# Kernel optimization log

Measured on AMD Instinct MI355X. Metric: run time of the kernel, lower is better.

The kernel has to match this reference:

```python
import jax, jax.numpy as jnp
import numpy as np

BLOCK_SIZE = 16
# Signed NVFP4 (e2m1) value table; code = sign_bit<<3 | magnitude_index
FP4_VALUES = jnp.array(
    [0.0, 0.5, 1.0, 1.5, 2.0, 3.0, 4.0, 6.0,
     -0.0, -0.5, -1.0, -1.5, -2.0, -3.0, -4.0, -6.0],
    dtype=jnp.float32)


def setup_inputs() -> dict:
    key = jax.random.key(0)
    k1, k2, k3 = jax.random.split(key, 3)
    O, I = 4096, 4096
    x = jax.random.normal(k1, (2, 1024, I), dtype=jnp.float32)
    # per-block scales (positive), one per 16-element block along in_features
    weight_scales = jax.random.uniform(k2, (O, I // BLOCK_SIZE), dtype=jnp.float32,
                                       minval=0.01, maxval=1.0)
    weight_q = jax.random.randint(k3, (O, I), 0, 16, dtype=jnp.int32)
    return {"x": x, "weight_scales": weight_scales, "weight_q": weight_q}


def dequantize_nvfp4_sim(weight_q, weight_scales, block_size=BLOCK_SIZE):
    O, I = weight_q.shape
    vals = FP4_VALUES[weight_q]                              # [O, I] fp32 e2m1 values
    w = vals.reshape(O, I // block_size, block_size) * weight_scales[:, :, None]
    return w.reshape(O, I)


def reference(x, weight_scales, weight_q):
    # Dequantize NVFP4 -> BF16, then BF16 GEMM (F.linear), cast back to input dtype.
    w = dequantize_nvfp4_sim(weight_q, weight_scales).astype(jnp.bfloat16)  # [O, I]
    x_bf16 = x.astype(jnp.bfloat16)
    out = jnp.einsum('bsi,oi->bso', x_bf16, w)               # [B, S, O] bf16
    return out.astype(x.dtype)
```

## Files before the change

kernel.cpp:

```cpp
#include <hip/hip_runtime.h>

typedef __bf16  bf16x8 __attribute__((ext_vector_type(8)));
typedef float   f32x4  __attribute__((ext_vector_type(4)));
typedef short   short8 __attribute__((ext_vector_type(8)));

static __device__ __forceinline__ unsigned short f2bf(float f) {
  union { float f; unsigned int u; } v; v.f = f;
  unsigned int u = v.u;
  u += 0x7fffu + ((u >> 16) & 1u);
  return (unsigned short)(u >> 16);
}

static __device__ __forceinline__ float fp4_decode(int qc) {
  int e = (qc >> 1) & 3;
  float m = (float)(qc & 1);
  float mag = (e == 0) ? (0.5f * m)
                       : ((2.0f + m) * 0.5f * (float)(1 << (e - 1)));
  return (qc & 8) ? -mag : mag;
}

__global__ __launch_bounds__(256) void w4a16_prep(
    const int* __restrict__ wq, const float* __restrict__ wsc,
    short* __restrict__ wout, int nblkW,
    const float* __restrict__ x, short* __restrict__ xb, int n8) {
  const int nbW = nblkW >> 8;
  if ((int)blockIdx.x < nbW) {
    int idx = blockIdx.x * 256 + threadIdx.x;
    if (idx >= nblkW) return;
    float s = wsc[idx];
    const int4* qp = (const int4*)wq + (size_t)idx * 4;
    int4 q0 = qp[0], q1 = qp[1], q2 = qp[2], q3 = qp[3];
    short8 r0, r1;
    r0[0] = (short)f2bf(fp4_decode(q0.x) * s);
    r0[1] = (short)f2bf(fp4_decode(q0.y) * s);
    r0[2] = (short)f2bf(fp4_decode(q0.z) * s);
    r0[3] = (short)f2bf(fp4_decode(q0.w) * s);
    r0[4] = (short)f2bf(fp4_decode(q1.x) * s);
    r0[5] = (short)f2bf(fp4_decode(q1.y) * s);
    r0[6] = (short)f2bf(fp4_decode(q1.z) * s);
    r0[7] = (short)f2bf(fp4_decode(q1.w) * s);
    r1[0] = (short)f2bf(fp4_decode(q2.x) * s);
    r1[1] = (short)f2bf(fp4_decode(q2.y) * s);
    r1[2] = (short)f2bf(fp4_decode(q2.z) * s);
    r1[3] = (short)f2bf(fp4_decode(q2.w) * s);
    r1[4] = (short)f2bf(fp4_decode(q3.x) * s);
    r1[5] = (short)f2bf(fp4_decode(q3.y) * s);
    r1[6] = (short)f2bf(fp4_decode(q3.z) * s);
    r1[7] = (short)f2bf(fp4_decode(q3.w) * s);
    short8* op = (short8*)wout + (size_t)idx * 2;
    op[0] = r0;
    op[1] = r1;
  } else {
    int idx = (blockIdx.x - nbW) * 256 + threadIdx.x;
    if (idx >= n8) return;
    const float4* xp = (const float4*)x + (size_t)idx * 2;
    float4 a = xp[0], b = xp[1];
    short8 r;
    r[0] = (short)f2bf(a.x); r[1] = (short)f2bf(a.y);
    r[2] = (short)f2bf(a.z); r[3] = (short)f2bf(a.w);
    r[4] = (short)f2bf(b.x); r[5] = (short)f2bf(b.y);
    r[6] = (short)f2bf(b.z); r[7] = (short)f2bf(b.w);
    ((short8*)xb)[idx] = r;
  }
}

#define BM 128
#define BN 256
#define BK 64
#define NBUF 3
#define ASZ (BM * BK)
#define BSZ (BN * BK)

__global__ __launch_bounds__(512, 2) void w4a16_gemm_1ph(
    const short* __restrict__ A, const short* __restrict__ B,
    float* __restrict__ C, int M, int N, int K) {
  __shared__ __attribute__((aligned(16))) short As[NBUF * ASZ];
  __shared__ __attribute__((aligned(16))) short Bs[NBUF * BSZ];

  const int tid  = threadIdx.x;
  const int lane = tid & 63;
  const int wid  = tid >> 6;
  const int wr   = wid >> 2;
  const int wc   = wid & 3;

  const int bm = blockIdx.y * BM;
  const int bn = blockIdx.x * BN;

  f32x4 acc[4][4] = {};

  const int fr    = lane & 15;
  const int klane = lane >> 4;
  const int xv    = fr & 7;

  const size_t rowbytes = (size_t)K * 2;

  size_t aoff[2];  int aldso[2];
#pragma unroll
  for (int r = 0; r < 2; ++r) {
    int u = r * 512 + tid;
    int row = u >> 3, c = u & 7;
    int csrc = c ^ (row & 7);
    aoff[r]  = (size_t)(bm + row) * rowbytes + (size_t)csrc * 16;
    aldso[r] = u * 16;
  }
  size_t boff[4];  int bldso[4];
#pragma unroll
  for (int r = 0; r < 4; ++r) {
    int u = r * 512 + tid;
    int row = u >> 3, c = u & 7;
    int csrc = c ^ (row & 7);
    boff[r]  = (size_t)(bn + row) * rowbytes + (size_t)csrc * 16;
    bldso[r] = u * 16;
  }

  const char* Ag = (const char*)A;
  const char* Bg = (const char*)B;

#define STAGE_A(bufbase, koff2, r)                                              \
  __builtin_amdgcn_global_load_lds(                                             \
      (const __attribute__((address_space(1))) unsigned int*)(Ag + aoff[r] + (koff2)), \
      (__attribute__((address_space(3))) unsigned int*)((char*)(bufbase) + aldso[r]),  \
      16, 0, 0)
#define STAGE_B(bufbase, koff2, r)                                              \
  __builtin_amdgcn_global_load_lds(                                             \
      (const __attribute__((address_space(1))) unsigned int*)(Bg + boff[r] + (koff2)), \
      (__attribute__((address_space(3))) unsigned int*)((char*)(bufbase) + bldso[r]),  \
      16, 0, 0)

  auto readA = [&](const short* Ab, int mq, int mi, int kk) -> bf16x8 {
    int row = wr * 64 + mq * 32 + mi * 16 + fr;
    int c = kk * 4 + klane;
    return *(const bf16x8*)((const char*)Ab + (size_t)row * 128 + ((c ^ xv) << 4));
  };
  auto readB = [&](const short* Bb, int ni, int kk) -> bf16x8 {
    int row = wc * 64 + ni * 16 + fr;
    int c = kk * 4 + klane;
    return *(const bf16x8*)((const char*)Bb + (size_t)row * 128 + ((c ^ xv) << 4));
  };

  const int NT = K / BK;

  {
    char* A0 = (char*)As; char* B0 = (char*)Bs;
    char* A1 = (char*)(As + ASZ); char* B1 = (char*)(Bs + BSZ);
    STAGE_A(A0, 0, 0); STAGE_A(A0, 0, 1);
    STAGE_B(B0, 0, 0); STAGE_B(B0, 0, 1); STAGE_B(B0, 0, 2); STAGE_B(B0, 0, 3);
    size_t k2 = (size_t)BK * 2;
    STAGE_A(A1, k2, 0); STAGE_A(A1, k2, 1);
    STAGE_B(B1, k2, 0); STAGE_B(B1, k2, 1); STAGE_B(B1, k2, 2); STAGE_B(B1, k2, 3);
  }
  asm volatile("s_waitcnt vmcnt(6)");
  __builtin_amdgcn_s_barrier();

  int cur = 0, nxt = 2;
  for (int t = 0; t < NT; ++t) {
    const short* Ab = As + cur * ASZ;
    const short* Bb = Bs + cur * BSZ;
    char* An = (char*)(As + nxt * ASZ);
    char* Bn = (char*)(Bs + nxt * BSZ);
    const size_t koff2 = (size_t)(t + 2) * (BK * 2);
    const bool pf = (t + 2) < NT;

    bf16x8 af0[2][2], bfr[4][2], af1[2][2];

#pragma unroll
    for (int mi = 0; mi < 2; ++mi)
#pragma unroll
      for (int kk = 0; kk < 2; ++kk)
        af0[mi][kk] = readA(Ab, 0, mi, kk);
#pragma unroll
    for (int ni = 0; ni < 4; ++ni)
#pragma unroll
      for (int kk = 0; kk < 2; ++kk)
        bfr[ni][kk] = readB(Bb, ni, kk);
#pragma unroll
    for (int mi = 0; mi < 2; ++mi)
#pragma unroll
      for (int kk = 0; kk < 2; ++kk)
        af1[mi][kk] = readA(Ab, 1, mi, kk);

    if (pf) {
      STAGE_A(An, koff2, 0); STAGE_A(An, koff2, 1);
      STAGE_B(Bn, koff2, 0); STAGE_B(Bn, koff2, 1);
      STAGE_B(Bn, koff2, 2); STAGE_B(Bn, koff2, 3);
    }

    __builtin_amdgcn_s_setprio(1);
#pragma unroll
    for (int mi = 0; mi < 2; ++mi)
#pragma unroll
      for (int ni = 0; ni < 4; ++ni)
#pragma unroll
        for (int kk = 0; kk < 2; ++kk)
          acc[mi][ni] = __builtin_amdgcn_mfma_f32_16x16x32_bf16(
              af0[mi][kk], bfr[ni][kk], acc[mi][ni], 0, 0, 0);
#pragma unroll
    for (int mi = 0; mi < 2; ++mi)
#pragma unroll
      for (int ni = 0; ni < 4; ++ni)
#pragma unroll
        for (int kk = 0; kk < 2; ++kk)
          acc[2 + mi][ni] = __builtin_amdgcn_mfma_f32_16x16x32_bf16(
              af1[mi][kk], bfr[ni][kk], acc[2 + mi][ni], 0, 0, 0);
    __builtin_amdgcn_s_setprio(0);

    if (t < NT - 1) {
      __builtin_amdgcn_sched_barrier(0);
      if (pf) asm volatile("s_waitcnt vmcnt(6)");
      else    asm volatile("s_waitcnt vmcnt(0)");
    }
    __builtin_amdgcn_s_barrier();

    cur = (cur == NBUF - 1) ? 0 : cur + 1;
    nxt = (nxt == NBUF - 1) ? 0 : nxt + 1;
  }

  const int cn = lane & 15;
  const int rb = (lane >> 4) * 4;
#pragma unroll
  for (int ai = 0; ai < 4; ++ai)
#pragma unroll
    for (int bj = 0; bj < 4; ++bj) {
      int m0 = bm + wr * 64 + ai * 16 + rb;
      int n0 = bn + wc * 64 + bj * 16 + cn;
#pragma unroll
      for (int r = 0; r < 4; ++r)
        C[(size_t)(m0 + r) * N + n0] = acc[ai][bj][r];
    }
}

extern "C" void kernel_launch(void* const* d_in, const int* in_sizes, int n_in,
                              void* d_out, int out_size, void* d_ws, size_t ws_size,
                              hipStream_t stream) {
  const float* x   = (const float*)d_in[0];
  const float* wsc = (const float*)d_in[1];
  const int*   wq  = (const int*)d_in[2];
  float* out = (float*)d_out;

  const int K = 4096;
  const int N = in_sizes[2] / K;
  const int M = in_sizes[0] / K;

  short* Wb = (short*)d_ws;
  short* Xb = Wb + (size_t)N * K;

  int nblkW = (N * K) / 16;
  int n8    = (M * K) / 8;
  int gridP = (nblkW >> 8) + ((n8 + 255) >> 8);
  w4a16_prep<<<gridP, 256, 0, stream>>>(wq, wsc, Wb, nblkW, x, Xb, n8);

  dim3 grid(N / BN, M / BM);
  w4a16_gemm_1ph<<<grid, 512, 0, stream>>>(Xb, Wb, out, M, N, K);
}
```

Measured before the change: 90.93 us.

## Load A fragments directly into registers and double-buffer only B in LDS

The activation operand A is no longer staged through shared memory. Each wave loads its A fragments straight from global memory into registers, ping-ponging between two register sets one tile ahead. Only the weight operand B stays in LDS, now double-buffered instead of triple-buffered, and the main loop is unrolled by two to alternate buffers. This saves LDS traffic and capacity for A, at the cost of redundant A loads across the four waves that share rows, poorly coalesced 16-byte row-strided global reads, shallower B prefetch, and higher register pressure.

Result: slower. 179.2 us (+97.1%).

```diff
diff --git a/kernel.cpp b/kernel.cpp
--- a/kernel.cpp
+++ b/kernel.cpp
@@ -67,15 +67,12 @@
 #define BM 128
 #define BN 256
 #define BK 64
-#define NBUF 3
-#define ASZ (BM * BK)
 #define BSZ (BN * BK)
 
-__global__ __launch_bounds__(512, 2) void w4a16_gemm_1ph(
+__global__ __launch_bounds__(512, 2) void w4a16_gemm_areg(
     const short* __restrict__ A, const short* __restrict__ B,
     float* __restrict__ C, int M, int N, int K) {
-  __shared__ __attribute__((aligned(16))) short As[NBUF * ASZ];
-  __shared__ __attribute__((aligned(16))) short Bs[NBUF * BSZ];
+  __shared__ __attribute__((aligned(16))) short Bs[2 * BSZ];
 
   const int tid  = threadIdx.x;
   const int lane = tid & 63;
@@ -94,15 +91,6 @@
 
   const size_t rowbytes = (size_t)K * 2;
 
-  size_t aoff[2];  int aldso[2];
-#pragma unroll
-  for (int r = 0; r < 2; ++r) {
-    int u = r * 512 + tid;
-    int row = u >> 3, c = u & 7;
-    int csrc = c ^ (row & 7);
-    aoff[r]  = (size_t)(bm + row) * rowbytes + (size_t)csrc * 16;
-    aldso[r] = u * 16;
-  }
   size_t boff[4];  int bldso[4];
 #pragma unroll
   for (int r = 0; r < 4; ++r) {
@@ -112,26 +100,21 @@
     boff[r]  = (size_t)(bn + row) * rowbytes + (size_t)csrc * 16;
     bldso[r] = u * 16;
   }
-
-  const char* Ag = (const char*)A;
   const char* Bg = (const char*)B;
 
-#define STAGE_A(bufbase, koff2, r)                                              \
-  __builtin_amdgcn_global_load_lds(                                             \
-      (const __attribute__((address_space(1))) unsigned int*)(Ag + aoff[r] + (koff2)), \
-      (__attribute__((address_space(3))) unsigned int*)((char*)(bufbase) + aldso[r]),  \
-      16, 0, 0)
 #define STAGE_B(bufbase, koff2, r)                                              \
   __builtin_amdgcn_global_load_lds(                                             \
       (const __attribute__((address_space(1))) unsigned int*)(Bg + boff[r] + (koff2)), \
       (__attribute__((address_space(3))) unsigned int*)((char*)(bufbase) + bldso[r]),  \
       16, 0, 0)
 
-  auto readA = [&](const short* Ab, int mq, int mi, int kk) -> bf16x8 {
-    int row = wr * 64 + mq * 32 + mi * 16 + fr;
-    int c = kk * 4 + klane;
-    return *(const bf16x8*)((const char*)Ab + (size_t)row * 128 + ((c ^ xv) << 4));
-  };
+  const char* Apl[4];
+#pragma unroll
+  for (int mi = 0; mi < 4; ++mi) {
+    int row = bm + wr * 64 + mi * 16 + fr;
+    Apl[mi] = (const char*)A + (size_t)row * rowbytes + klane * 16;
+  }
+
   auto readB = [&](const short* Bb, int ni, int kk) -> bf16x8 {
     int row = wc * 64 + ni * 16 + fr;
     int c = kk * 4 + klane;
@@ -139,80 +122,56 @@
   };
 
   const int NT = K / BK;
-
-  {
-    char* A0 = (char*)As; char* B0 = (char*)Bs;
-    char* A1 = (char*)(As + ASZ); char* B1 = (char*)(Bs + BSZ);
-    STAGE_A(A0, 0, 0); STAGE_A(A0, 0, 1);
-    STAGE_B(B0, 0, 0); STAGE_B(B0, 0, 1); STAGE_B(B0, 0, 2); STAGE_B(B0, 0, 3);
-    size_t k2 = (size_t)BK * 2;
-    STAGE_A(A1, k2, 0); STAGE_A(A1, k2, 1);
-    STAGE_B(B1, k2, 0); STAGE_B(B1, k2, 1); STAGE_B(B1, k2, 2); STAGE_B(B1, k2, 3);
-  }
-  asm volatile("s_waitcnt vmcnt(6)");
+  short* Bs0 = Bs;
+  short* Bs1 = Bs + BSZ;
+
+  bf16x8 bfr[4][2], afA[4][2], afB[4][2];
+
+  STAGE_B(Bs0, 0, 0); STAGE_B(Bs0, 0, 1); STAGE_B(Bs0, 0, 2); STAGE_B(Bs0, 0, 3);
+  __builtin_amdgcn_sched_barrier(0);
+#pragma unroll
+  for (int mi = 0; mi < 4; ++mi)
+#pragma unroll
+    for (int kk = 0; kk < 2; ++kk)
+      afA[mi][kk] = *(const bf16x8*)(Apl[mi] + kk * 64);
+  __builtin_amdgcn_sched_barrier(0);
+  asm volatile("s_waitcnt vmcnt(8)");
   __builtin_amdgcn_s_barrier();
 
-  int cur = 0, nxt = 2;
-  for (int t = 0; t < NT; ++t) {
-    const short* Ab = As + cur * ASZ;
-    const short* Bb = Bs + cur * BSZ;
-    char* An = (char*)(As + nxt * ASZ);
-    char* Bn = (char*)(Bs + nxt * BSZ);
-    const size_t koff2 = (size_t)(t + 2) * (BK * 2);
-    const bool pf = (t + 2) < NT;
-
-    bf16x8 af0[2][2], bfr[4][2], af1[2][2];
-
-#pragma unroll
-    for (int mi = 0; mi < 2; ++mi)
-#pragma unroll
-      for (int kk = 0; kk < 2; ++kk)
-        af0[mi][kk] = readA(Ab, 0, mi, kk);
-#pragma unroll
-    for (int ni = 0; ni < 4; ++ni)
-#pragma unroll
-      for (int kk = 0; kk < 2; ++kk)
-        bfr[ni][kk] = readB(Bb, ni, kk);
-#pragma unroll
-    for (int mi = 0; mi < 2; ++mi)
-#pragma unroll
-      for (int kk = 0; kk < 2; ++kk)
-        af1[mi][kk] = readA(Ab, 1, mi, kk);
-
-    if (pf) {
-      STAGE_A(An, koff2, 0); STAGE_A(An, koff2, 1);
-      STAGE_B(Bn, koff2, 0); STAGE_B(Bn, koff2, 1);
-      STAGE_B(Bn, koff2, 2); STAGE_B(Bn, koff2, 3);
-    }
-
-    __builtin_amdgcn_s_setprio(1);
-#pragma unroll
-    for (int mi = 0; mi < 2; ++mi)
-#pragma unroll
-      for (int ni = 0; ni < 4; ++ni)
-#pragma unroll
-        for (int kk = 0; kk < 2; ++kk)
-          acc[mi][ni] = __builtin_amdgcn_mfma_f32_16x16x32_bf16(
-              af0[mi][kk], bfr[ni][kk], acc[mi][ni], 0, 0, 0);
-#pragma unroll
-    for (int mi = 0; mi < 2; ++mi)
-#pragma unroll
-      for (int ni = 0; ni < 4; ++ni)
-#pragma unroll
-        for (int kk = 0; kk < 2; ++kk)
-          acc[2 + mi][ni] = __builtin_amdgcn_mfma_f32_16x16x32_bf16(
-              af1[mi][kk], bfr[ni][kk], acc[2 + mi][ni], 0, 0, 0);
-    __builtin_amdgcn_s_setprio(0);
-
-    if (t < NT - 1) {
-      __builtin_amdgcn_sched_barrier(0);
-      if (pf) asm volatile("s_waitcnt vmcnt(6)");
-      else    asm volatile("s_waitcnt vmcnt(0)");
-    }
-    __builtin_amdgcn_s_barrier();
-
-    cur = (cur == NBUF - 1) ? 0 : cur + 1;
-    nxt = (nxt == NBUF - 1) ? 0 : nxt + 1;
+#define TILE_BODY(t_, CURB, NXTB, AFU, AFL)                                     \
+  do {                                                                          \
+    _Pragma("unroll") for (int ni = 0; ni < 4; ++ni)                            \
+      _Pragma("unroll") for (int kk = 0; kk < 2; ++kk)                          \
+        bfr[ni][kk] = readB((CURB), ni, kk);                                    \
+    const bool pf_ = (t_) + 1 < NT;                                             \
+    if (pf_) {                                                                  \
+      const size_t ko_ = (size_t)((t_) + 1) * (BK * 2);                         \
+      STAGE_B((NXTB), ko_, 0); STAGE_B((NXTB), ko_, 1);                         \
+      STAGE_B((NXTB), ko_, 2); STAGE_B((NXTB), ko_, 3);                         \
+    }                                                                           \
+    __builtin_amdgcn_sched_barrier(0);  \
+    if (pf_) {                                                                  \
+      _Pragma("unroll") for (int mi = 0; mi < 4; ++mi)                          \
+        _Pragma("unroll") for (int kk = 0; kk < 2; ++kk)                        \
+          AFL[mi][kk] = *(const bf16x8*)(Apl[mi] + ((t_) + 1) * 128 + kk * 64); \
+    }                                                                           \
+    __builtin_amdgcn_s_setprio(1);                                              \
+    _Pragma("unroll") for (int mi = 0; mi < 4; ++mi)                            \
+      _Pragma("unroll") for (int ni = 0; ni < 4; ++ni)                          \
+        _Pragma("unroll") for (int kk = 0; kk < 2; ++kk)                        \
+          acc[mi][ni] = __builtin_amdgcn_mfma_f32_16x16x32_bf16(                \
+              AFU[mi][kk], bfr[ni][kk], acc[mi][ni], 0, 0, 0);                  \
+    __builtin_amdgcn_s_setprio(0);                                              \
+    if ((t_) < NT - 1) {                                                        \
+      __builtin_amdgcn_sched_barrier(0);                                        \
+      asm volatile("s_waitcnt vmcnt(8)");    \
+      __builtin_amdgcn_s_barrier();                                             \
+    }                                                                           \
+  } while (0)
+
+  for (int t = 0; t < NT; t += 2) {
+    TILE_BODY(t,     Bs0, Bs1, afA, afB);
+    TILE_BODY(t + 1, Bs1, Bs0, afB, afA);
   }
 
   const int cn = lane & 15;
@@ -250,5 +209,5 @@
   w4a16_prep<<<gridP, 256, 0, stream>>>(wq, wsc, Wb, nblkW, x, Xb, n8);
 
   dim3 grid(N / BN, M / BM);
-  w4a16_gemm_1ph<<<grid, 512, 0, stream>>>(Xb, Wb, out, M, N, K);
-}
+  w4a16_gemm_areg<<<grid, 512, 0, stream>>>(Xb, Wb, out, M, N, K);
+}
```

## Shrink GEMM tiles to 128x128x32 with 4 waves for higher occupancy

Applied to the files above, without the earlier changes.

Reduces the GEMM block tile from 128x256x64 with 8 waves to 128x128x32 with 4 waves, targeting three blocks per CU instead of two. The LDS swizzle and fragment-read pattern are rewritten for 64-byte rows, and each K step now issues 16 MFMAs per wave instead of 32. This is meant to raise occupancy and produce more blocks to fill the CUs, at the cost of less data reuse per tile, twice as many barriers per K, and more global traffic for A.

Measured after the change: 101.3 us. +11.5%, slower.

```diff
diff --git a/kernel.cpp b/kernel.cpp
--- a/kernel.cpp
+++ b/kernel.cpp
@@ -65,13 +65,13 @@
 }
 
 #define BM 128
-#define BN 256
-#define BK 64
+#define BN 128
+#define BK 32
 #define NBUF 3
 #define ASZ (BM * BK)
 #define BSZ (BN * BK)
 
-__global__ __launch_bounds__(512, 2) void w4a16_gemm_1ph(
+__global__ __launch_bounds__(256, 3) void w4a16_gemm_occ(
     const short* __restrict__ A, const short* __restrict__ B,
     float* __restrict__ C, int M, int N, int K) {
   __shared__ __attribute__((aligned(16))) short As[NBUF * ASZ];
@@ -80,8 +80,8 @@
   const int tid  = threadIdx.x;
   const int lane = tid & 63;
   const int wid  = tid >> 6;
-  const int wr   = wid >> 2;
-  const int wc   = wid & 3;
+  const int wr   = wid >> 1;
+  const int wc   = wid & 1;
 
   const int bm = blockIdx.y * BM;
   const int bn = blockIdx.x * BN;
@@ -90,66 +90,55 @@
 
   const int fr    = lane & 15;
   const int klane = lane >> 4;
-  const int xv    = fr & 7;
+  const int xk    = klane ^ ((fr >> 1) & 3);
 
   const size_t rowbytes = (size_t)K * 2;
 
-  size_t aoff[2];  int aldso[2];
+  size_t aoff[2], boff[2];  int ldso[2];
 #pragma unroll
   for (int r = 0; r < 2; ++r) {
-    int u = r * 512 + tid;
-    int row = u >> 3, c = u & 7;
-    int csrc = c ^ (row & 7);
-    aoff[r]  = (size_t)(bm + row) * rowbytes + (size_t)csrc * 16;
-    aldso[r] = u * 16;
-  }
-  size_t boff[4];  int bldso[4];
-#pragma unroll
-  for (int r = 0; r < 4; ++r) {
-    int u = r * 512 + tid;
-    int row = u >> 3, c = u & 7;
-    int csrc = c ^ (row & 7);
-    boff[r]  = (size_t)(bn + row) * rowbytes + (size_t)csrc * 16;
-    bldso[r] = u * 16;
-  }
-
+    int u = r * 256 + tid;
+    int row = u >> 2, c = u & 3;
+    int csrc = c ^ ((row >> 1) & 3);
+    aoff[r] = (size_t)(bm + row) * rowbytes + (size_t)csrc * 16;
+    boff[r] = (size_t)(bn + row) * rowbytes + (size_t)csrc * 16;
+    ldso[r] = u * 16;
+  }
   const char* Ag = (const char*)A;
   const char* Bg = (const char*)B;
 
 #define STAGE_A(bufbase, koff2, r)                                              \
   __builtin_amdgcn_global_load_lds(                                             \
       (const __attribute__((address_space(1))) unsigned int*)(Ag + aoff[r] + (koff2)), \
-      (__attribute__((address_space(3))) unsigned int*)((char*)(bufbase) + aldso[r]),  \
+      (__attribute__((address_space(3))) unsigned int*)((char*)(bufbase) + ldso[r]),   \
       16, 0, 0)
 #define STAGE_B(bufbase, koff2, r)                                              \
   __builtin_amdgcn_global_load_lds(                                             \
       (const __attribute__((address_space(1))) unsigned int*)(Bg + boff[r] + (koff2)), \
-      (__attribute__((address_space(3))) unsigned int*)((char*)(bufbase) + bldso[r]),  \
+      (__attribute__((address_space(3))) unsigned int*)((char*)(bufbase) + ldso[r]),   \
       16, 0, 0)
 
-  auto readA = [&](const short* Ab, int mq, int mi, int kk) -> bf16x8 {
-    int row = wr * 64 + mq * 32 + mi * 16 + fr;
-    int c = kk * 4 + klane;
-    return *(const bf16x8*)((const char*)Ab + (size_t)row * 128 + ((c ^ xv) << 4));
+  auto readA = [&](const short* Ab, int mi) -> bf16x8 {
+    int row = wr * 64 + mi * 16 + fr;
+    return *(const bf16x8*)((const char*)Ab + (size_t)row * 64 + (xk << 4));
   };
-  auto readB = [&](const short* Bb, int ni, int kk) -> bf16x8 {
+  auto readB = [&](const short* Bb, int ni) -> bf16x8 {
     int row = wc * 64 + ni * 16 + fr;
-    int c = kk * 4 + klane;
-    return *(const bf16x8*)((const char*)Bb + (size_t)row * 128 + ((c ^ xv) << 4));
+    return *(const bf16x8*)((const char*)Bb + (size_t)row * 64 + (xk << 4));
   };
 
   const int NT = K / BK;
 
   {
-    char* A0 = (char*)As; char* B0 = (char*)Bs;
-    char* A1 = (char*)(As + ASZ); char* B1 = (char*)(Bs + BSZ);
+    char* A0 = (char*)As;            char* B0 = (char*)Bs;
+    char* A1 = (char*)(As + ASZ);    char* B1 = (char*)(Bs + BSZ);
     STAGE_A(A0, 0, 0); STAGE_A(A0, 0, 1);
-    STAGE_B(B0, 0, 0); STAGE_B(B0, 0, 1); STAGE_B(B0, 0, 2); STAGE_B(B0, 0, 3);
+    STAGE_B(B0, 0, 0); STAGE_B(B0, 0, 1);
     size_t k2 = (size_t)BK * 2;
     STAGE_A(A1, k2, 0); STAGE_A(A1, k2, 1);
-    STAGE_B(B1, k2, 0); STAGE_B(B1, k2, 1); STAGE_B(B1, k2, 2); STAGE_B(B1, k2, 3);
-  }
-  asm volatile("s_waitcnt vmcnt(6)");
+    STAGE_B(B1, k2, 0); STAGE_B(B1, k2, 1);
+  }
+  asm volatile("s_waitcnt vmcnt(4)");
   __builtin_amdgcn_s_barrier();
 
   int cur = 0, nxt = 2;
@@ -161,52 +150,29 @@
     const size_t koff2 = (size_t)(t + 2) * (BK * 2);
     const bool pf = (t + 2) < NT;
 
-    bf16x8 af0[2][2], bfr[4][2], af1[2][2];
-
-#pragma unroll
-    for (int mi = 0; mi < 2; ++mi)
-#pragma unroll
-      for (int kk = 0; kk < 2; ++kk)
-        af0[mi][kk] = readA(Ab, 0, mi, kk);
-#pragma unroll
-    for (int ni = 0; ni < 4; ++ni)
-#pragma unroll
-      for (int kk = 0; kk < 2; ++kk)
-        bfr[ni][kk] = readB(Bb, ni, kk);
-#pragma unroll
-    for (int mi = 0; mi < 2; ++mi)
-#pragma unroll
-      for (int kk = 0; kk < 2; ++kk)
-        af1[mi][kk] = readA(Ab, 1, mi, kk);
+    bf16x8 af[4], bf[4];
+#pragma unroll
+    for (int mi = 0; mi < 4; ++mi) af[mi] = readA(Ab, mi);
+#pragma unroll
+    for (int ni = 0; ni < 4; ++ni) bf[ni] = readB(Bb, ni);
 
     if (pf) {
       STAGE_A(An, koff2, 0); STAGE_A(An, koff2, 1);
       STAGE_B(Bn, koff2, 0); STAGE_B(Bn, koff2, 1);
-      STAGE_B(Bn, koff2, 2); STAGE_B(Bn, koff2, 3);
     }
 
     __builtin_amdgcn_s_setprio(1);
 #pragma unroll
-    for (int mi = 0; mi < 2; ++mi)
+    for (int mi = 0; mi < 4; ++mi)
 #pragma unroll
       for (int ni = 0; ni < 4; ++ni)
-#pragma unroll
-        for (int kk = 0; kk < 2; ++kk)
-          acc[mi][ni] = __builtin_amdgcn_mfma_f32_16x16x32_bf16(
-              af0[mi][kk], bfr[ni][kk], acc[mi][ni], 0, 0, 0);
-#pragma unroll
-    for (int mi = 0; mi < 2; ++mi)
-#pragma unroll
-      for (int ni = 0; ni < 4; ++ni)
-#pragma unroll
-        for (int kk = 0; kk < 2; ++kk)
-          acc[2 + mi][ni] = __builtin_amdgcn_mfma_f32_16x16x32_bf16(
-              af1[mi][kk], bfr[ni][kk], acc[2 + mi][ni], 0, 0, 0);
+        acc[mi][ni] = __builtin_amdgcn_mfma_f32_16x16x32_bf16(
+            af[mi], bf[ni], acc[mi][ni], 0, 0, 0);
     __builtin_amdgcn_s_setprio(0);
 
     if (t < NT - 1) {
       __builtin_amdgcn_sched_barrier(0);
-      if (pf) asm volatile("s_waitcnt vmcnt(6)");
+      if (pf) asm volatile("s_waitcnt vmcnt(4)");
       else    asm volatile("s_waitcnt vmcnt(0)");
     }
     __builtin_amdgcn_s_barrier();
@@ -250,5 +216,5 @@
   w4a16_prep<<<gridP, 256, 0, stream>>>(wq, wsc, Wb, nblkW, x, Xb, n8);
 
   dim3 grid(N / BN, M / BM);
-  w4a16_gemm_1ph<<<grid, 512, 0, stream>>>(Xb, Wb, out, M, N, K);
-}
+  w4a16_gemm_occ<<<grid, 256, 0, stream>>>(Xb, Wb, out, M, N, K);
+}
```

## Double-buffer LDS fragments in registers and overlap reads with MFMA halves

Applied to the files above, without the earlier changes.

Restructures the GEMM main loop so the next K-tile's A/B fragments are read from LDS into a second register set between the two halves of the MFMA work, ping-ponging between two fragment sets via a manually unrolled pair of tile bodies. The barrier now sits mid-tile, so LDS reads overlap with the second half of the MFMAs instead of stalling before compute. To hold the doubled fragment registers, launch bounds drop to one block per CU, which risks lower occupancy and less latency hiding across waves.

Result: no change. 90.07 us (-0.9%).

```diff
diff --git a/kernel.cpp b/kernel.cpp
--- a/kernel.cpp
+++ b/kernel.cpp
@@ -71,7 +71,7 @@
 #define ASZ (BM * BK)
 #define BSZ (BN * BK)
 
-__global__ __launch_bounds__(512, 2) void w4a16_gemm_1ph(
+__global__ __launch_bounds__(512, 1) void w4a16_gemm_ra(
     const short* __restrict__ A, const short* __restrict__ B,
     float* __restrict__ C, int M, int N, int K) {
   __shared__ __attribute__((aligned(16))) short As[NBUF * ASZ];
@@ -127,8 +127,8 @@
       (__attribute__((address_space(3))) unsigned int*)((char*)(bufbase) + bldso[r]),  \
       16, 0, 0)
 
-  auto readA = [&](const short* Ab, int mq, int mi, int kk) -> bf16x8 {
-    int row = wr * 64 + mq * 32 + mi * 16 + fr;
+  auto readA = [&](const short* Ab, int mi, int kk) -> bf16x8 {
+    int row = wr * 64 + mi * 16 + fr;
     int c = kk * 4 + klane;
     return *(const bf16x8*)((const char*)Ab + (size_t)row * 128 + ((c ^ xv) << 4));
   };
@@ -140,6 +140,8 @@
 
   const int NT = K / BK;
 
+  bf16x8 afA[4][2], bfA[4][2], afB[4][2], bfB[4][2];
+
   {
     char* A0 = (char*)As; char* B0 = (char*)Bs;
     char* A1 = (char*)(As + ASZ); char* B1 = (char*)(Bs + BSZ);
@@ -149,70 +151,69 @@
     STAGE_A(A1, k2, 0); STAGE_A(A1, k2, 1);
     STAGE_B(B1, k2, 0); STAGE_B(B1, k2, 1); STAGE_B(B1, k2, 2); STAGE_B(B1, k2, 3);
   }
+  __builtin_amdgcn_sched_barrier(0);
   asm volatile("s_waitcnt vmcnt(6)");
   __builtin_amdgcn_s_barrier();
-
-  int cur = 0, nxt = 2;
-  for (int t = 0; t < NT; ++t) {
-    const short* Ab = As + cur * ASZ;
-    const short* Bb = Bs + cur * BSZ;
-    char* An = (char*)(As + nxt * ASZ);
-    char* Bn = (char*)(Bs + nxt * BSZ);
-    const size_t koff2 = (size_t)(t + 2) * (BK * 2);
-    const bool pf = (t + 2) < NT;
-
-    bf16x8 af0[2][2], bfr[4][2], af1[2][2];
-
-#pragma unroll
-    for (int mi = 0; mi < 2; ++mi)
-#pragma unroll
-      for (int kk = 0; kk < 2; ++kk)
-        af0[mi][kk] = readA(Ab, 0, mi, kk);
-#pragma unroll
-    for (int ni = 0; ni < 4; ++ni)
-#pragma unroll
-      for (int kk = 0; kk < 2; ++kk)
-        bfr[ni][kk] = readB(Bb, ni, kk);
-#pragma unroll
-    for (int mi = 0; mi < 2; ++mi)
-#pragma unroll
-      for (int kk = 0; kk < 2; ++kk)
-        af1[mi][kk] = readA(Ab, 1, mi, kk);
-
-    if (pf) {
-      STAGE_A(An, koff2, 0); STAGE_A(An, koff2, 1);
-      STAGE_B(Bn, koff2, 0); STAGE_B(Bn, koff2, 1);
-      STAGE_B(Bn, koff2, 2); STAGE_B(Bn, koff2, 3);
-    }
-
-    __builtin_amdgcn_s_setprio(1);
-#pragma unroll
-    for (int mi = 0; mi < 2; ++mi)
-#pragma unroll
-      for (int ni = 0; ni < 4; ++ni)
-#pragma unroll
-        for (int kk = 0; kk < 2; ++kk)
-          acc[mi][ni] = __builtin_amdgcn_mfma_f32_16x16x32_bf16(
-              af0[mi][kk], bfr[ni][kk], acc[mi][ni], 0, 0, 0);
-#pragma unroll
-    for (int mi = 0; mi < 2; ++mi)
-#pragma unroll
-      for (int ni = 0; ni < 4; ++ni)
-#pragma unroll
-        for (int kk = 0; kk < 2; ++kk)
-          acc[2 + mi][ni] = __builtin_amdgcn_mfma_f32_16x16x32_bf16(
-              af1[mi][kk], bfr[ni][kk], acc[2 + mi][ni], 0, 0, 0);
-    __builtin_amdgcn_s_setprio(0);
-
-    if (t < NT - 1) {
-      __builtin_amdgcn_sched_barrier(0);
-      if (pf) asm volatile("s_waitcnt vmcnt(6)");
-      else    asm volatile("s_waitcnt vmcnt(0)");
-    }
-    __builtin_amdgcn_s_barrier();
-
-    cur = (cur == NBUF - 1) ? 0 : cur + 1;
-    nxt = (nxt == NBUF - 1) ? 0 : nxt + 1;
+  __builtin_amdgcn_sched_barrier(0);
+#pragma unroll
+  for (int mi = 0; mi < 4; ++mi)
+#pragma unroll
+    for (int kk = 0; kk < 2; ++kk)
+      afA[mi][kk] = readA(As, mi, kk);
+#pragma unroll
+  for (int ni = 0; ni < 4; ++ni)
+#pragma unroll
+    for (int kk = 0; kk < 2; ++kk)
+      bfA[ni][kk] = readB(Bs, ni, kk);
+
+  int nr = 1, ns = 2;
+
+#define TILE_BODY(t_, AFU, BFU, AFL, BFL)                                       \
+  do {                                                                          \
+    if ((t_) + 2 < NT) {                                                        \
+      char* An = (char*)(As + ns * ASZ);                                        \
+      char* Bn = (char*)(Bs + ns * BSZ);                                        \
+      const size_t ko_ = (size_t)((t_) + 2) * (BK * 2);                         \
+      STAGE_A(An, ko_, 0); STAGE_A(An, ko_, 1);                                 \
+      STAGE_B(Bn, ko_, 0); STAGE_B(Bn, ko_, 1);                                 \
+      STAGE_B(Bn, ko_, 2); STAGE_B(Bn, ko_, 3);                                 \
+    }                                                                           \
+    __builtin_amdgcn_s_setprio(1);                                              \
+    _Pragma("unroll") for (int mi = 0; mi < 2; ++mi)                            \
+      _Pragma("unroll") for (int ni = 0; ni < 4; ++ni)                          \
+        _Pragma("unroll") for (int kk = 0; kk < 2; ++kk)                        \
+          acc[mi][ni] = __builtin_amdgcn_mfma_f32_16x16x32_bf16(                \
+              AFU[mi][kk], BFU[ni][kk], acc[mi][ni], 0, 0, 0);                  \
+    __builtin_amdgcn_s_setprio(0);                                              \
+    __builtin_amdgcn_sched_barrier(0);                                          \
+    if ((t_) + 1 < NT) {                                                        \
+      if ((t_) + 2 < NT) asm volatile("s_waitcnt vmcnt(6)");                    \
+      else               asm volatile("s_waitcnt vmcnt(0)");                    \
+      __builtin_amdgcn_s_barrier();                       \
+      __builtin_amdgcn_sched_barrier(0);                                        \
+      const short* Ar = As + nr * ASZ;                                          \
+      const short* Br = Bs + nr * BSZ;                                          \
+      _Pragma("unroll") for (int mi = 0; mi < 4; ++mi)                          \
+        _Pragma("unroll") for (int kk = 0; kk < 2; ++kk)                        \
+          AFL[mi][kk] = readA(Ar, mi, kk);                                      \
+      _Pragma("unroll") for (int ni = 0; ni < 4; ++ni)                          \
+        _Pragma("unroll") for (int kk = 0; kk < 2; ++kk)                        \
+          BFL[ni][kk] = readB(Br, ni, kk);                                      \
+      __builtin_amdgcn_sched_barrier(0);                                        \
+    }                                                                           \
+    __builtin_amdgcn_s_setprio(1);                                              \
+    _Pragma("unroll") for (int mi = 2; mi < 4; ++mi)                            \
+      _Pragma("unroll") for (int ni = 0; ni < 4; ++ni)                          \
+        _Pragma("unroll") for (int kk = 0; kk < 2; ++kk)                        \
+          acc[mi][ni] = __builtin_amdgcn_mfma_f32_16x16x32_bf16(                \
+              AFU[mi][kk], BFU[ni][kk], acc[mi][ni], 0, 0, 0);                  \
+    __builtin_amdgcn_s_setprio(0);                                              \
+    nr = ns; ns = (ns == NBUF - 1) ? 0 : ns + 1;                                \
+  } while (0)
+
+  for (int t = 0; t < NT; t += 2) {
+    TILE_BODY(t,     afA, bfA, afB, bfB);
+    TILE_BODY(t + 1, afB, bfB, afA, bfA);
   }
 
   const int cn = lane & 15;
@@ -250,5 +251,5 @@
   w4a16_prep<<<gridP, 256, 0, stream>>>(wq, wsc, Wb, nblkW, x, Xb, n8);
 
   dim3 grid(N / BN, M / BM);
-  w4a16_gemm_1ph<<<grid, 512, 0, stream>>>(Xb, Wb, out, M, N, K);
-}
+  w4a16_gemm_ra<<<grid, 512, 0, stream>>>(Xb, Wb, out, M, N, K);
+}
```
